# Kernel tuning notes

Measured on AMD Instinct MI355X. Metric: run time of the kernel, lower is better.

## Reference

```python
import jax, jax.numpy as jnp
import numpy as np

DIM = 384
DH = 32
H = DIM // DH          # 12 heads
N_WIN = 3072           # total windows
W_ACT = 1536           # active windows = M
T = 64                 # tokens per window (8x8)
NTOK = W_ACT * T       # 98304 active tokens
N_BLOCK = 9830
MLP = 4 * DIM
EPS = 1e-5


def _layer_norm(h, w, b):
    mu = jnp.mean(h, axis=-1, keepdims=True)
    var = jnp.mean(jnp.square(h - mu), axis=-1, keepdims=True)
    return (h - mu) * jax.lax.rsqrt(var + EPS) * w + b


def setup_inputs() -> dict:
    key = jax.random.key(0)
    ks = jax.random.split(key, 16)
    x = jax.random.normal(ks[0], (N_WIN, T, DIM), jnp.float32)
    # unique active windows, sorted (scatter-restore requires uniqueness)
    index_window = jnp.sort(jax.random.permutation(ks[1], N_WIN)[:W_ACT])
    # full permutation of active tokens into M groups of size S
    index_partition = jax.random.permutation(ks[2], NTOK)
    blocked_index = jax.random.permutation(ks[3], NTOK)[:N_BLOCK]
    s = 0.02
    params = dict(
        ln1_w=jnp.ones((DIM,), jnp.float32), ln1_b=jnp.zeros((DIM,), jnp.float32),
        qkv_w=jax.random.normal(ks[4], (3 * DIM, DIM), jnp.float32) * s,
        qkv_b=jnp.zeros((3 * DIM,), jnp.float32),
        proj_w=jax.random.normal(ks[5], (DIM, DIM), jnp.float32) * s,
        proj_b=jnp.zeros((DIM,), jnp.float32),
        ln2_w=jnp.ones((DIM,), jnp.float32), ln2_b=jnp.zeros((DIM,), jnp.float32),
        fc1_w=jax.random.normal(ks[6], (MLP, DIM), jnp.float32) * s,
        fc1_b=jnp.zeros((MLP,), jnp.float32),
        fc2_w=jax.random.normal(ks[7], (DIM, MLP), jnp.float32) * s,
        fc2_b=jnp.zeros((DIM,), jnp.float32),
    )
    return dict(x=x, index_window=index_window, index_partition=index_partition,
                blocked_index=blocked_index, M=W_ACT, K=jnp.zeros((1,), jnp.int64),
                **params)


def reference(x, index_window, index_partition, blocked_index, M, K,
              ln1_w, ln1_b, qkv_w, qkv_b, proj_w, proj_b,
              ln2_w, ln2_b, fc1_w, fc1_b, fc2_w, fc2_b):
    N, T_, C = x.shape
    scale = DH ** -0.5
    S = index_partition.shape[0] // M

    xn = _layer_norm(x, ln1_w, ln1_b)                      # (N, T, C)
    xw = xn[index_window].reshape(-1, C)                   # (NTOK, C) active tokens
    xp = xw[index_partition].reshape(M, S, C)              # (M, S, C) regrouped
    shortcut = xp

    qkv = (xp @ qkv_w.T + qkv_b).reshape(M, S, H, 3 * DH)  # per-head [q|k|v] chunks
    q, k, v = qkv[..., :DH], qkv[..., DH:2 * DH], qkv[..., 2 * DH:]

    attn = jnp.einsum('mqhd,mkhd->mhqk', q, k) * scale     # (M, H, Sq, Sk)

    # scatter scores into full-size map keyed by KEY token, mask blocked keys, gather back
    amap = jnp.zeros((xw.shape[0], S, H), attn.dtype)      # (NTOK, Sq, H)
    amap = amap.at[index_partition].set(jnp.transpose(attn, (0, 3, 2, 1)).reshape(-1, S, H))
    amap = amap.at[blocked_index].set(-10000.0)
    attn = jnp.transpose(amap[index_partition].reshape(M, S, S, H), (0, 3, 2, 1))
    attn = jax.nn.softmax(attn, axis=-1)

    o = jnp.einsum('mhqk,mkhd->mqhd', attn, v).reshape(M, S, C)
    o = o @ proj_w.T + proj_b

    # sub_layers: [Id, Id(+res), LN, fc1, GELU, fc2(+res)]
    h = shortcut + o
    shortcut = h
    h2 = _layer_norm(h, ln2_w, ln2_b)
    h2 = jax.nn.gelu(h2 @ fc1_w.T + fc1_b, approximate=False)
    h = shortcut + (h2 @ fc2_w.T + fc2_b)

    # scatter-restore: blocked tokens keep their (normed) input values
    XX = xw.at[index_partition].set(h.reshape(-1, C))
    XX = XX.at[blocked_index].set(xw[blocked_index])
    out = xn.at[index_window].set(XX.reshape(M, -1, C))
    return out
```

## Files before the change

### kernel.cpp

```cpp
#include <hip/hip_runtime.h>
#include <hip/hip_bf16.h>

typedef __attribute__((ext_vector_type(8))) short bf16x8;
typedef __attribute__((ext_vector_type(4))) short s16x4;
typedef __attribute__((ext_vector_type(4))) float f32x4;
typedef __attribute__((ext_vector_type(2))) long longx2;
typedef __attribute__((ext_vector_type(16))) unsigned char u8x16;

#define NW_   3072
#define WACT_ 1536
#define NTOK_ 98304
#define NBLK_ 9830
#define DIM_  384
#define QKVD_ 1152
#define MLPD_ 1536

__device__ __forceinline__ float bf2f(short s) {
  union { unsigned u; float f; } c;
  c.u = ((unsigned)(unsigned short)s) << 16;
  return c.f;
}
__device__ __forceinline__ short f2bf(float f) {
  union { float f; unsigned u; } c; c.f = f;
  unsigned lsb = (c.u >> 16) & 1u;
  c.u += 0x7fffu + lsb;
  return (short)(c.u >> 16);
}

__device__ __forceinline__ f32x4 mfma16(bf16x8 a, bf16x8 b, f32x4 c) {
  return __builtin_amdgcn_mfma_f32_16x16x32_bf16(a, b, c, 0, 0, 0);
}
__device__ __forceinline__ f32x4 mfma8(long a, long b, f32x4 c) {
  return __builtin_amdgcn_mfma_f32_16x16x32_fp8_fp8(a, b, c, 0, 0, 0);
}

__device__ __forceinline__ void gload16(const void* g, void* l) {
  __builtin_amdgcn_global_load_lds(
      (const __attribute__((address_space(1))) unsigned*)g,
      (__attribute__((address_space(3))) unsigned*)l, 16, 0, 0);
}

__global__ __launch_bounds__(256) void mapA_k(int* win_rank, unsigned* bitmap) {
  int t = blockIdx.x * 256 + threadIdx.x;
  if (t < NW_) { win_rank[t] = -1; bitmap[t] = 0u; }
}

__global__ __launch_bounds__(256) void mapB_k(const int* __restrict__ iw,
                                              const int* __restrict__ blk,
                                              int* win_rank, unsigned* bitmap) {
  int t = blockIdx.x * 256 + threadIdx.x;
  if (t < WACT_) win_rank[iw[t]] = t;
  if (t < NBLK_) { int j = blk[t]; atomicOr(&bitmap[j >> 5], 1u << (j & 31)); }
}

__global__ __launch_bounds__(256) void mapC_k(const int* __restrict__ ip,
                                              const int* __restrict__ iw,
                                              const unsigned* __restrict__ bitmap,
                                              int* inv_ip, int* rowmap) {
  int i = blockIdx.x * 256 + threadIdx.x;
  if (i < NTOK_) {
    int j = ip[i];
    inv_ip[j] = i;
    int blocked = (bitmap[j >> 5] >> (j & 31)) & 1;
    rowmap[i] = blocked ? -1 : (iw[j >> 6] * 64 + (j & 63));
  }
}

__global__ __launch_bounds__(256) void wconv_k(const float* __restrict__ qkvw,
                                               const float* __restrict__ projw,
                                               const float* __restrict__ fc1w,
                                               short* __restrict__ dst) {
  int i = (blockIdx.x * 256 + threadIdx.x) * 4;
  f32x4 v;
  if (i < 442368) v = *(const f32x4*)&qkvw[i];
  else if (i < 589824) v = *(const f32x4*)&projw[i - 442368];
  else v = *(const f32x4*)&fc1w[i - 589824];
  s16x4 o;
#pragma unroll
  for (int e = 0; e < 4; ++e) o[e] = f2bf(v[e]);
  *(s16x4*)&dst[i] = o;
}

__global__ __launch_bounds__(256) void wconv8_k(const float* __restrict__ fc2w,
                                                unsigned char* __restrict__ dst) {
  int i = (blockIdx.x * 256 + threadIdx.x) * 8;
  f32x4 v0 = *(const f32x4*)&fc2w[i];
  f32x4 v1 = *(const f32x4*)&fc2w[i + 4];
  int w0 = __builtin_amdgcn_cvt_pk_fp8_f32(v0[0], v0[1], 0, false);
  w0 = __builtin_amdgcn_cvt_pk_fp8_f32(v0[2], v0[3], w0, true);
  int w1 = __builtin_amdgcn_cvt_pk_fp8_f32(v1[0], v1[1], 0, false);
  w1 = __builtin_amdgcn_cvt_pk_fp8_f32(v1[2], v1[3], w1, true);
  int kro = i % MLPD_, row = i / MLPD_;
  int g = kro >> 6, l = (kro >> 3) & 7;
  int s = ((l & 3) << 1) | (l >> 2);
  union { int u[2]; long ll; } p; p.u[0] = w0; p.u[1] = w1;
  *(long*)&dst[(size_t)row * MLPD_ + g * 64 + s * 8] = p.ll;
}

__global__ __launch_bounds__(256) void ln1_k(const float* __restrict__ x,
                                             const float* __restrict__ w,
                                             const float* __restrict__ b,
                                             const int* __restrict__ win_rank,
                                             const int* __restrict__ inv_ip,
                                             const unsigned* __restrict__ bitmap,
                                             float* __restrict__ out,
                                             short* __restrict__ xp) {
  const int l = threadIdx.x & 31;
  const int tok = blockIdx.x * 8 + (threadIdx.x >> 5);
  const f32x4* xr = (const f32x4*)(x + (size_t)tok * DIM_);
  f32x4 v[3]; float s = 0.f;
#pragma unroll
  for (int j = 0; j < 3; ++j) {
    v[j] = xr[l + 32 * j];
    s += v[j][0] + v[j][1] + v[j][2] + v[j][3];
  }
#pragma unroll
  for (int m = 1; m <= 16; m <<= 1) s += __shfl_xor(s, m, 64);
  float mu = s * (1.0f / DIM_);
  float q = 0.f;
#pragma unroll
  for (int j = 0; j < 3; ++j)
#pragma unroll
    for (int e = 0; e < 4; ++e) { float d = v[j][e] - mu; q += d * d; }
#pragma unroll
  for (int m = 1; m <= 16; m <<= 1) q += __shfl_xor(q, m, 64);
  float rs = rsqrtf(q * (1.0f / DIM_) + 1e-5f);
  f32x4 y[3];
#pragma unroll
  for (int j = 0; j < 3; ++j) {
    f32x4 wv = *(const f32x4*)&w[4 * l + 128 * j];
    f32x4 bv = *(const f32x4*)&b[4 * l + 128 * j];
#pragma unroll
    for (int e = 0; e < 4; ++e) y[j][e] = (v[j][e] - mu) * rs * wv[e] + bv[e];
  }
  int wdw = tok >> 6, t = tok & 63;
  int rank = win_rank[wdw];
  if (rank < 0) {
    f32x4* po = (f32x4*)(out + (size_t)tok * DIM_);
#pragma unroll
    for (int j = 0; j < 3; ++j) po[l + 32 * j] = y[j];
  } else {
    int jdx = (rank << 6) + t;
    int i = inv_ip[jdx];
#pragma unroll
    for (int j = 0; j < 3; ++j) {
      s16x4 o;
#pragma unroll
      for (int e = 0; e < 4; ++e) o[e] = f2bf(y[j][e]);
      *(s16x4*)&xp[(size_t)i * DIM_ + 4 * l + 128 * j] = o;
    }
    if ((bitmap[jdx >> 5] >> (jdx & 31)) & 1) {
      f32x4* po = (f32x4*)(out + (size_t)tok * DIM_);
#pragma unroll
      for (int j = 0; j < 3; ++j) po[l + 32 * j] = y[j];
    }
  }
}

__global__ __launch_bounds__(256) void ln2_k(const short* __restrict__ h,
                                             const float* __restrict__ w,
                                             const float* __restrict__ b,
                                             short* __restrict__ outln) {
  const int l = threadIdx.x & 31;
  const int tok = blockIdx.x * 8 + (threadIdx.x >> 5);
  const s16x4* xr = (const s16x4*)(h + (size_t)tok * DIM_);
  float v[12]; float s = 0.f;
#pragma unroll
  for (int j = 0; j < 3; ++j) {
    s16x4 rv = xr[l + 32 * j];
#pragma unroll
    for (int e = 0; e < 4; ++e) { v[j * 4 + e] = bf2f(rv[e]); s += v[j * 4 + e]; }
  }
#pragma unroll
  for (int m = 1; m <= 16; m <<= 1) s += __shfl_xor(s, m, 64);
  float mu = s * (1.0f / DIM_);
  float q = 0.f;
#pragma unroll
  for (int e = 0; e < 12; ++e) { float d = v[e] - mu; q += d * d; }
#pragma unroll
  for (int m = 1; m <= 16; m <<= 1) q += __shfl_xor(q, m, 64);
  float rs = rsqrtf(q * (1.0f / DIM_) + 1e-5f);
  s16x4* po = (s16x4*)(outln + (size_t)tok * DIM_);
#pragma unroll
  for (int j = 0; j < 3; ++j) {
    f32x4 wv = *(const f32x4*)&w[4 * l + 128 * j];
    f32x4 bv = *(const f32x4*)&b[4 * l + 128 * j];
    s16x4 o;
#pragma unroll
    for (int e = 0; e < 4; ++e)
      o[e] = f2bf((v[j * 4 + e] - mu) * rs * wv[e] + bv[e]);
    po[l + 32 * j] = o;
  }
}

template <int EPI>
__global__ __launch_bounds__(512) void gemm_k(const short* __restrict__ A,
                                              const short* __restrict__ B,
                                              const float* __restrict__ bias,
                                              int K, int N, int nx,
                                              unsigned char* __restrict__ C8) {
  const int nwg = gridDim.x;
  const int q8 = nwg >> 3;
  const int wg = (blockIdx.x & 7) * q8 + (blockIdx.x >> 3);
  const int ntile = wg % nx, mtile = wg / nx;
  const int tid = threadIdx.x, wid = tid >> 6, lane = tid & 63;
  const int fq = lane >> 4, fr = lane & 15;
  const int wr = wid >> 1, wc = wid & 1;
  __shared__ __align__(16) short lA[256 * 64];
  __shared__ __align__(16) short lB[128 * 64];
  const int row0 = mtile * 256, col0 = ntile * 128;
  float bs[4];
#pragma unroll
  for (int nt = 0; nt < 4; ++nt) bs[nt] = bias[col0 + wc * 64 + nt * 16 + fr];
  f32x4 acc[4][4];
#pragma unroll
  for (int a = 0; a < 4; ++a)
#pragma unroll
    for (int c = 0; c < 4; ++c) acc[a][c] = (f32x4){0.f, 0.f, 0.f, 0.f};
  const int nkt = K >> 6;
  for (int kt = 0; kt < nkt; ++kt) {
    const int k0 = kt << 6;
#pragma unroll
    for (int i = 0; i < 4; ++i) {
      int g = i * 512 + tid;
      int r = g >> 3, c8 = g & 7;
      int s8 = c8 ^ (r & 7);
      gload16(A + (size_t)(row0 + r) * K + k0 + s8 * 8, (char*)lA + (size_t)g * 16);
    }
#pragma unroll
    for (int i = 0; i < 2; ++i) {
      int g = i * 512 + tid;
      int r = g >> 3, c8 = g & 7;
      int s8 = c8 ^ (r & 7);
      gload16(B + (size_t)(col0 + r) * K + k0 + s8 * 8, (char*)lB + (size_t)g * 16);
    }
    __syncthreads();
#pragma unroll
    for (int ks = 0; ks < 2; ++ks) {
      bf16x8 af[4], bfr[4];
#pragma unroll
      for (int mt = 0; mt < 4; ++mt) {
        int r = wr * 64 + mt * 16 + fr;
        af[mt] = *(const bf16x8*)&lA[r * 64 + ((ks * 4 + fq) ^ (r & 7)) * 8];
      }
#pragma unroll
      for (int nt = 0; nt < 4; ++nt) {
        int r = wc * 64 + nt * 16 + fr;
        bfr[nt] = *(const bf16x8*)&lB[r * 64 + ((ks * 4 + fq) ^ (r & 7)) * 8];
      }
#pragma unroll
      for (int mt = 0; mt < 4; ++mt)
#pragma unroll
        for (int nt = 0; nt < 4; ++nt)
          acc[mt][nt] = mfma16(af[mt], bfr[nt], acc[mt][nt]);
    }
    __syncthreads();
  }
#pragma unroll
  for (int mt = 0; mt < 4; ++mt) {
#pragma unroll
    for (int jj = 0; jj < 4; ++jj) {
      int r = row0 + wr * 64 + mt * 16 + fq * 4 + jj;
      if (EPI == 0) {
        float g4[4];
#pragma unroll
        for (int nt = 0; nt < 4; ++nt) g4[nt] = acc[mt][nt][jj] + bs[nt];
        int p01 = __builtin_amdgcn_cvt_pk_fp8_f32(g4[0], g4[1], 0, false);
        int p23 = __builtin_amdgcn_cvt_pk_fp8_f32(g4[2], g4[3], 0, false);
        const size_t rb = (size_t)r * N + col0 + wc * 64 + fr;
        C8[rb]      = (unsigned char)(p01 & 0xff);
        C8[rb + 16] = (unsigned char)((p01 >> 8) & 0xff);
        C8[rb + 32] = (unsigned char)(p23 & 0xff);
        C8[rb + 48] = (unsigned char)((p23 >> 8) & 0xff);
      } else {
        float g4[4];
#pragma unroll
        for (int nt = 0; nt < 4; ++nt) {
          float v = acc[mt][nt][jj] + bs[nt];
          float u = v * (0.79788456f + 0.03567741f * v * v);
          g4[nt] = v * __builtin_amdgcn_rcpf(1.0f + __expf(-2.0f * u));
        }
        int p01 = __builtin_amdgcn_cvt_pk_fp8_f32(g4[0], g4[1], 0, false);
        int p23 = __builtin_amdgcn_cvt_pk_fp8_f32(g4[2], g4[3], 0, false);
        const int C0 = col0 + wc * 64;
        const size_t rb = (size_t)r * MLPD_ + C0 + (fr & 7) + ((fr >> 3) << 4);
        C8[rb]      = (unsigned char)(p01 & 0xff);
        C8[rb + 32] = (unsigned char)((p01 >> 8) & 0xff);
        C8[rb + 8]  = (unsigned char)(p23 & 0xff);
        C8[rb + 40] = (unsigned char)((p23 >> 8) & 0xff);
      }
    }
  }
}

__global__ __launch_bounds__(256) void gemm128_k(const short* __restrict__ A,
                                                 const short* __restrict__ B,
                                                 const float* __restrict__ bias,
                                                 int K, int nx,
                                                 short* __restrict__ Cb,
                                                 const short* __restrict__ add_bf) {
  const int nwg = gridDim.x;
  const int q8 = nwg >> 3;
  const int wg = (blockIdx.x & 7) * q8 + (blockIdx.x >> 3);
  const int ntile = wg % nx, mtile = wg / nx;
  const int tid = threadIdx.x, wid = tid >> 6, lane = tid & 63;
  const int fq = lane >> 4, fr = lane & 15;
  const int wr = wid >> 1, wc = wid & 1;
  __shared__ __align__(16) short lA[128 * 64];
  __shared__ __align__(16) short lB[128 * 64];
  const int row0 = mtile * 128, col0 = ntile * 128;
  float bs[4];
#pragma unroll
  for (int nt = 0; nt < 4; ++nt) bs[nt] = bias[col0 + wc * 64 + nt * 16 + fr];
  f32x4 acc[4][4];
#pragma unroll
  for (int a = 0; a < 4; ++a)
#pragma unroll
    for (int c = 0; c < 4; ++c) acc[a][c] = (f32x4){0.f, 0.f, 0.f, 0.f};
  const int nkt = K >> 6;
  for (int kt = 0; kt < nkt; ++kt) {
    const int k0 = kt << 6;
#pragma unroll
    for (int i = 0; i < 4; ++i) {
      int cb = ((i * 4 + wid) << 6) + lane;
      int r = cb >> 3, c8 = cb & 7;
      int s8 = c8 ^ (r & 7);
      gload16(A + (size_t)(row0 + r) * K + k0 + s8 * 8,
              (char*)lA + (size_t)(i * 4 + wid) * 1024);
      gload16(B + (size_t)(col0 + r) * K + k0 + s8 * 8,
              (char*)lB + (size_t)(i * 4 + wid) * 1024);
    }
    __syncthreads();
#pragma unroll
    for (int ks = 0; ks < 2; ++ks) {
      bf16x8 af[4], bfr[4];
#pragma unroll
      for (int mt = 0; mt < 4; ++mt) {
        int r = wr * 64 + mt * 16 + fr;
        af[mt] = *(const bf16x8*)&lA[r * 64 + ((ks * 4 + fq) ^ (r & 7)) * 8];
      }
#pragma unroll
      for (int nt = 0; nt < 4; ++nt) {
        int r = wc * 64 + nt * 16 + fr;
        bfr[nt] = *(const bf16x8*)&lB[r * 64 + ((ks * 4 + fq) ^ (r & 7)) * 8];
      }
#pragma unroll
      for (int mt = 0; mt < 4; ++mt)
#pragma unroll
        for (int nt = 0; nt < 4; ++nt)
          acc[mt][nt] = mfma16(af[mt], bfr[nt], acc[mt][nt]);
    }
    __syncthreads();
  }
#pragma unroll
  for (int mt = 0; mt < 4; ++mt) {
#pragma unroll
    for (int jj = 0; jj < 4; ++jj) {
      int r = row0 + wr * 64 + mt * 16 + fq * 4 + jj;
#pragma unroll
      for (int nt = 0; nt < 4; ++nt) {
        int gcol = col0 + wc * 64 + nt * 16 + fr;
        float v = acc[mt][nt][jj] + bs[nt] + bf2f(add_bf[(size_t)r * DIM_ + gcol]);
        Cb[(size_t)r * DIM_ + gcol] = f2bf(v);
      }
    }
  }
}

__global__ __launch_bounds__(256) void gemmf8_k(const unsigned char* __restrict__ A8,
                                                const unsigned char* __restrict__ B8,
                                                const float* __restrict__ bias,
                                                int nx,
                                                const short* __restrict__ add_bf,
                                                const int* __restrict__ rowmap,
                                                float* __restrict__ outf) {
  const int K = MLPD_;
  const int nwg = gridDim.x;
  const int q8 = nwg >> 3;
  const int wg = (blockIdx.x & 7) * q8 + (blockIdx.x >> 3);
  const int ntile = wg % nx, mtile = wg / nx;
  const int tid = threadIdx.x, wid = tid >> 6, lane = tid & 63;
  const int fq = lane >> 4, fr = lane & 15;
  const int wr = wid >> 1, wc = wid & 1;
  __shared__ __align__(16) unsigned char lA[128 * 128];
  __shared__ __align__(16) unsigned char lB[128 * 128];
  const int row0 = mtile * 128, col0 = ntile * 128;
  float bs[4];
#pragma unroll
  for (int nt = 0; nt < 4; ++nt) bs[nt] = bias[col0 + wc * 64 + nt * 16 + fr];
  f32x4 acc[4][4];
#pragma unroll
  for (int a = 0; a < 4; ++a)
#pragma unroll
    for (int c = 0; c < 4; ++c) acc[a][c] = (f32x4){0.f, 0.f, 0.f, 0.f};
  const int nkt = K >> 7;
  for (int kt = 0; kt < nkt; ++kt) {
    const int k0 = kt << 7;
#pragma unroll
    for (int i = 0; i < 4; ++i) {
      int g = i * 256 + tid;
      int r = g >> 3, c8 = g & 7;
      int s8 = c8 ^ (r & 7);
      gload16(A8 + (size_t)(row0 + r) * K + k0 + s8 * 16, (char*)lA + (size_t)g * 16);
      gload16(B8 + (size_t)(col0 + r) * K + k0 + s8 * 16, (char*)lB + (size_t)g * 16);
    }
    __syncthreads();
#pragma unroll
    for (int ss = 0; ss < 2; ++ss) {
      longx2 af[4], bfr[4];
      const int pb = ss * 4 + fq;
#pragma unroll
      for (int mt = 0; mt < 4; ++mt) {
        int r = wr * 64 + mt * 16 + fr;
        int d = pb ^ (r & 7);
        af[mt] = *(const longx2*)&lA[r * 128 + d * 16];
      }
#pragma unroll
      for (int nt = 0; nt < 4; ++nt) {
        int r = wc * 64 + nt * 16 + fr;
        int d = pb ^ (r & 7);
        bfr[nt] = *(const longx2*)&lB[r * 128 + d * 16];
      }
#pragma unroll
      for (int mt = 0; mt < 4; ++mt)
#pragma unroll
        for (int nt = 0; nt < 4; ++nt) {
          acc[mt][nt] = mfma8(af[mt][0], bfr[nt][0], acc[mt][nt]);
          acc[mt][nt] = mfma8(af[mt][1], bfr[nt][1], acc[mt][nt]);
        }
    }
    __syncthreads();
  }
#pragma unroll
  for (int mt = 0; mt < 4; ++mt) {
#pragma unroll
    for (int jj = 0; jj < 4; ++jj) {
      int r = row0 + wr * 64 + mt * 16 + fq * 4 + jj;
      int dmap = rowmap[r];
#pragma unroll
      for (int nt = 0; nt < 4; ++nt) {
        int gcol = col0 + wc * 64 + nt * 16 + fr;
        float v = acc[mt][nt][jj] + bs[nt] + bf2f(add_bf[(size_t)r * DIM_ + gcol]);
        if (dmap >= 0) outf[(size_t)dmap * DIM_ + gcol] = v;
      }
    }
  }
}

__global__ __launch_bounds__(256) void attn_k(const unsigned char* __restrict__ qkv8,
                                              const unsigned* __restrict__ bitmap,
                                              const int* __restrict__ ip,
                                              short* __restrict__ o) {
  const int flat = (blockIdx.x & 7) * 576 + (blockIdx.x >> 3);
  const int m = flat / 3;
  const int h = (flat % 3) * 4 + (threadIdx.x >> 6);
  const int wid = threadIdx.x >> 6, lane = threadIdx.x & 63;
  const int fq = lane >> 4, fr = lane & 15;
  __shared__ __align__(16) unsigned char P[4][64 * 72];
  __shared__ __align__(16) unsigned char Vt[4][32 * 72];
  __shared__ unsigned char flags[64];
  if (threadIdx.x < 64) {
    int j = ip[m * 64 + threadIdx.x];
    flags[threadIdx.x] = (unsigned char)((bitmap[j >> 5] >> (j & 31)) & 1);
  }
  __syncthreads();
  const float scale = 0.17677669529663687f;
  int msk[4];
#pragma unroll
  for (int nt = 0; nt < 4; ++nt) msk[nt] = flags[nt * 16 + fr];

  const unsigned char* base = qkv8 + (size_t)m * 64 * QKVD_ + h * 96;
  f32x4 sacc[4][4];
#pragma unroll
  for (int a = 0; a < 4; ++a)
#pragma unroll
    for (int c = 0; c < 4; ++c) sacc[a][c] = (f32x4){0.f, 0.f, 0.f, 0.f};
  long qa[4], kb[4];
#pragma unroll
  for (int mt = 0; mt < 4; ++mt)
    qa[mt] = *(const long*)(base + (size_t)(mt * 16 + fr) * QKVD_ + fq * 8);
#pragma unroll
  for (int nt = 0; nt < 4; ++nt)
    kb[nt] = *(const long*)(base + (size_t)(nt * 16 + fr) * QKVD_ + 32 + fq * 8);
#pragma unroll
  for (int mt = 0; mt < 4; ++mt)
#pragma unroll
    for (int nt = 0; nt < 4; ++nt)
      sacc[mt][nt] = mfma8(qa[mt], kb[nt], sacc[mt][nt]);
#pragma unroll
  for (int c = 0; c < 2; ++c) {
    u8x16 vv = *(const u8x16*)(base + (size_t)lane * QKVD_ + 64 + c * 16);
#pragma unroll
    for (int e = 0; e < 16; ++e) Vt[wid][(c * 16 + e) * 72 + lane] = vv[e];
  }
#pragma unroll
  for (int mt = 0; mt < 4; ++mt)
#pragma unroll
    for (int nt = 0; nt < 4; ++nt) {
      f32x4 sv = sacc[mt][nt];
#pragma unroll
      for (int jj = 0; jj < 4; ++jj)
        sv[jj] = msk[nt] ? -10000.0f : sv[jj] * scale;
      sacc[mt][nt] = sv;
    }
#pragma unroll
  for (int mt = 0; mt < 4; ++mt) {
#pragma unroll
    for (int jj = 0; jj < 4; ++jj) {
      float mx = sacc[mt][0][jj];
#pragma unroll
      for (int nt = 1; nt < 4; ++nt) mx = fmaxf(mx, sacc[mt][nt][jj]);
#pragma unroll
      for (int mm = 1; mm < 16; mm <<= 1) mx = fmaxf(mx, __shfl_xor(mx, mm, 64));
      float sm = 0.f;
      float p[4];
#pragma unroll
      for (int nt = 0; nt < 4; ++nt) {
        p[nt] = __expf(sacc[mt][nt][jj] - mx);
        sm += p[nt];
      }
#pragma unroll
      for (int mm = 1; mm < 16; mm <<= 1) sm += __shfl_xor(sm, mm, 64);
      float inv = 1.0f / sm;
      int rowb = (mt * 16 + fq * 4 + jj) * 72;
      int p01 = __builtin_amdgcn_cvt_pk_fp8_f32(p[0] * inv, p[1] * inv, 0, false);
      int p23 = __builtin_amdgcn_cvt_pk_fp8_f32(p[2] * inv, p[3] * inv, 0, false);
      P[wid][rowb + fr]      = (unsigned char)(p01 & 0xff);
      P[wid][rowb + 16 + fr] = (unsigned char)((p01 >> 8) & 0xff);
      P[wid][rowb + 32 + fr] = (unsigned char)(p23 & 0xff);
      P[wid][rowb + 48 + fr] = (unsigned char)((p23 >> 8) & 0xff);
    }
  }
  f32x4 oacc[4][2];
#pragma unroll
  for (int a = 0; a < 4; ++a)
#pragma unroll
    for (int c = 0; c < 2; ++c) oacc[a][c] = (f32x4){0.f, 0.f, 0.f, 0.f};
#pragma unroll
  for (int ks = 0; ks < 2; ++ks) {
    long pa[4], vb[2];
#pragma unroll
    for (int mt = 0; mt < 4; ++mt)
      pa[mt] = *(const long*)&P[wid][(mt * 16 + fr) * 72 + ks * 32 + fq * 8];
#pragma unroll
    for (int nd = 0; nd < 2; ++nd)
      vb[nd] = *(const long*)&Vt[wid][(nd * 16 + fr) * 72 + ks * 32 + fq * 8];
#pragma unroll
    for (int mt = 0; mt < 4; ++mt)
#pragma unroll
      for (int nd = 0; nd < 2; ++nd)
        oacc[mt][nd] = mfma8(pa[mt], vb[nd], oacc[mt][nd]);
  }
#pragma unroll
  for (int mt = 0; mt < 4; ++mt)
#pragma unroll
    for (int nd = 0; nd < 2; ++nd)
#pragma unroll
      for (int jj = 0; jj < 4; ++jj)
        o[(size_t)(m * 64 + mt * 16 + fq * 4 + jj) * DIM_ + h * 32 + nd * 16 + fr] =
            f2bf(oacc[mt][nd][jj]);
}

extern "C" void kernel_launch(void* const* d_in, const int* in_sizes, int n_in,
                              void* d_out, int out_size, void* d_ws, size_t ws_size,
                              hipStream_t stream) {
  const float* x = (const float*)d_in[0];
  const int* iw = (const int*)d_in[1];
  const int* ip = (const int*)d_in[2];
  const int* blk = (const int*)d_in[3];
  const float* ln1w = (const float*)d_in[6];
  const float* ln1b = (const float*)d_in[7];
  const float* qkvw = (const float*)d_in[8];
  const float* qkvb = (const float*)d_in[9];
  const float* projw = (const float*)d_in[10];
  const float* projb = (const float*)d_in[11];
  const float* ln2w = (const float*)d_in[12];
  const float* ln2b = (const float*)d_in[13];
  const float* fc1w = (const float*)d_in[14];
  const float* fc1b = (const float*)d_in[15];
  const float* fc2w = (const float*)d_in[16];
  const float* fc2b = (const float*)d_in[17];
  float* out = (float*)d_out;

  char* ws = (char*)d_ws;
  short* w_all = (short*)ws;
  short* w_qkv = w_all;
  short* w_proj = w_all + 442368;
  short* w_fc1 = w_all + 589824;
  int* inv_ip = (int*)(ws + 3538944);
  int* rowmap = inv_ip + NTOK_;
  int* win_rank = rowmap + NTOK_;
  unsigned* bitmap = (unsigned*)(win_rank + NW_);
  short* xp = (short*)(ws + 4349952);
  unsigned char* qkv8 = (unsigned char*)(ws + 4349952 + 75497472);
  unsigned char* t8 = qkv8;
  unsigned char* w2f8 = (unsigned char*)(ws + 306339840);
  short* obuf = (short*)(ws + 381837312);
  short* hbuf = (short*)(ws + 457334784);
  short* ln2buf = xp;
  (void)in_sizes; (void)n_in; (void)out_size; (void)ws_size;

  mapA_k<<<12, 256, 0, stream>>>(win_rank, bitmap);
  mapB_k<<<39, 256, 0, stream>>>(iw, blk, win_rank, bitmap);
  mapC_k<<<NTOK_ / 256, 256, 0, stream>>>(ip, iw, bitmap, inv_ip, rowmap);
  wconv_k<<<1152, 256, 0, stream>>>(qkvw, projw, fc1w, w_all);
  wconv8_k<<<288, 256, 0, stream>>>(fc2w, w2f8);
  ln1_k<<<(NW_ * 64) / 8, 256, 0, stream>>>(x, ln1w, ln1b, win_rank, inv_ip, bitmap,
                                            out, xp);
  gemm_k<0><<<384 * 9, 512, 0, stream>>>(xp, w_qkv, qkvb, 384, QKVD_, 9, qkv8);
  attn_k<<<WACT_ * 3, 256, 0, stream>>>(qkv8, bitmap, ip, obuf);
  gemm128_k<<<768 * 3, 256, 0, stream>>>(obuf, w_proj, projb, 384, 3, hbuf, xp);
  ln2_k<<<NTOK_ / 8, 256, 0, stream>>>(hbuf, ln2w, ln2b, ln2buf);
  gemm_k<2><<<384 * 12, 512, 0, stream>>>(ln2buf, w_fc1, fc1b, 384, MLPD_, 12, t8);
  gemmf8_k<<<768 * 3, 256, 0, stream>>>(t8, w2f8, fc2b, 3, hbuf, rowmap, out);
}
```

Baseline: 744.5 us.

## Switch proj and fc1 GEMMs to FP8 with permuted-K activations

Converts the projection and fc1 weights to FP8 with the K-permuted layout, and makes the attention output and LN2 output write FP8 in the same layout. The proj and fc1 GEMMs now use the shared FP8 128x128 GEMM template instead of the bf16 kernels. This halves operand bytes and uses the faster FP8 MFMA path, at the cost of lower precision on two more matmuls. The fc1 tiling changes from 256x128 with 512 threads to 128x128 with 256 threads.

```diff
diff --git a/kernel.cpp b/kernel.cpp
--- a/kernel.cpp
+++ b/kernel.cpp
@@ -38,6 +38,12 @@
   __builtin_amdgcn_global_load_lds(
       (const __attribute__((address_space(1))) unsigned*)g,
       (__attribute__((address_space(3))) unsigned*)l, 16, 0, 0);
+}
+
+__device__ __forceinline__ int kperm(int col) {
+  int l = (col >> 3) & 7;
+  int s = ((l & 3) << 1) | (l >> 2);
+  return (col & ~63) + s * 8 + (col & 7);
 }
 
 __global__ __launch_bounds__(256) void mapA_k(int* win_rank, unsigned* bitmap) {
@@ -67,34 +73,28 @@
 }
 
 __global__ __launch_bounds__(256) void wconv_k(const float* __restrict__ qkvw,
-                                               const float* __restrict__ projw,
-                                               const float* __restrict__ fc1w,
                                                short* __restrict__ dst) {
   int i = (blockIdx.x * 256 + threadIdx.x) * 4;
-  f32x4 v;
-  if (i < 442368) v = *(const f32x4*)&qkvw[i];
-  else if (i < 589824) v = *(const f32x4*)&projw[i - 442368];
-  else v = *(const f32x4*)&fc1w[i - 589824];
+  f32x4 v = *(const f32x4*)&qkvw[i];
   s16x4 o;
 #pragma unroll
   for (int e = 0; e < 4; ++e) o[e] = f2bf(v[e]);
   *(s16x4*)&dst[i] = o;
 }
 
-__global__ __launch_bounds__(256) void wconv8_k(const float* __restrict__ fc2w,
-                                                unsigned char* __restrict__ dst) {
+__global__ __launch_bounds__(256) void wconv8_k(const float* __restrict__ src,
+                                                unsigned char* __restrict__ dst,
+                                                int K) {
   int i = (blockIdx.x * 256 + threadIdx.x) * 8;
-  f32x4 v0 = *(const f32x4*)&fc2w[i];
-  f32x4 v1 = *(const f32x4*)&fc2w[i + 4];
+  f32x4 v0 = *(const f32x4*)&src[i];
+  f32x4 v1 = *(const f32x4*)&src[i + 4];
   int w0 = __builtin_amdgcn_cvt_pk_fp8_f32(v0[0], v0[1], 0, false);
   w0 = __builtin_amdgcn_cvt_pk_fp8_f32(v0[2], v0[3], w0, true);
   int w1 = __builtin_amdgcn_cvt_pk_fp8_f32(v1[0], v1[1], 0, false);
   w1 = __builtin_amdgcn_cvt_pk_fp8_f32(v1[2], v1[3], w1, true);
-  int kro = i % MLPD_, row = i / MLPD_;
-  int g = kro >> 6, l = (kro >> 3) & 7;
-  int s = ((l & 3) << 1) | (l >> 2);
+  int kro = i % K, row = i / K;
   union { int u[2]; long ll; } p; p.u[0] = w0; p.u[1] = w1;
-  *(long*)&dst[(size_t)row * MLPD_ + g * 64 + s * 8] = p.ll;
+  *(long*)&dst[(size_t)row * K + kperm(kro)] = p.ll;
 }
 
 __global__ __launch_bounds__(256) void ln1_k(const float* __restrict__ x,
@@ -160,7 +160,7 @@
 __global__ __launch_bounds__(256) void ln2_k(const short* __restrict__ h,
                                              const float* __restrict__ w,
                                              const float* __restrict__ b,
-                                             short* __restrict__ outln) {
+                                             unsigned char* __restrict__ out8) {
   const int l = threadIdx.x & 31;
   const int tok = blockIdx.x * 8 + (threadIdx.x >> 5);
   const s16x4* xr = (const s16x4*)(h + (size_t)tok * DIM_);
@@ -180,25 +180,26 @@
 #pragma unroll
   for (int m = 1; m <= 16; m <<= 1) q += __shfl_xor(q, m, 64);
   float rs = rsqrtf(q * (1.0f / DIM_) + 1e-5f);
-  s16x4* po = (s16x4*)(outln + (size_t)tok * DIM_);
 #pragma unroll
   for (int j = 0; j < 3; ++j) {
     f32x4 wv = *(const f32x4*)&w[4 * l + 128 * j];
     f32x4 bv = *(const f32x4*)&b[4 * l + 128 * j];
-    s16x4 o;
+    float y[4];
 #pragma unroll
     for (int e = 0; e < 4; ++e)
-      o[e] = f2bf((v[j * 4 + e] - mu) * rs * wv[e] + bv[e]);
-    po[l + 32 * j] = o;
-  }
-}
-
-template <int EPI>
-__global__ __launch_bounds__(512) void gemm_k(const short* __restrict__ A,
-                                              const short* __restrict__ B,
-                                              const float* __restrict__ bias,
-                                              int K, int N, int nx,
-                                              unsigned char* __restrict__ C8) {
+      y[e] = (v[j * 4 + e] - mu) * rs * wv[e] + bv[e];
+    int wrd = __builtin_amdgcn_cvt_pk_fp8_f32(y[0], y[1], 0, false);
+    wrd = __builtin_amdgcn_cvt_pk_fp8_f32(y[2], y[3], wrd, true);
+    int c0 = 4 * l + 128 * j;
+    *(unsigned*)&out8[(size_t)tok * DIM_ + kperm(c0)] = (unsigned)wrd;
+  }
+}
+
+__global__ __launch_bounds__(512) void gemmqkv_k(const short* __restrict__ A,
+                                                 const short* __restrict__ B,
+                                                 const float* __restrict__ bias,
+                                                 unsigned char* __restrict__ C8) {
+  const int K = 384, N = QKVD_, nx = 9;
   const int nwg = gridDim.x;
   const int q8 = nwg >> 3;
   const int wg = (blockIdx.x & 7) * q8 + (blockIdx.x >> 3);
@@ -261,18 +262,101 @@
 #pragma unroll
     for (int jj = 0; jj < 4; ++jj) {
       int r = row0 + wr * 64 + mt * 16 + fq * 4 + jj;
-      if (EPI == 0) {
-        float g4[4];
-#pragma unroll
-        for (int nt = 0; nt < 4; ++nt) g4[nt] = acc[mt][nt][jj] + bs[nt];
-        int p01 = __builtin_amdgcn_cvt_pk_fp8_f32(g4[0], g4[1], 0, false);
-        int p23 = __builtin_amdgcn_cvt_pk_fp8_f32(g4[2], g4[3], 0, false);
-        const size_t rb = (size_t)r * N + col0 + wc * 64 + fr;
-        C8[rb]      = (unsigned char)(p01 & 0xff);
-        C8[rb + 16] = (unsigned char)((p01 >> 8) & 0xff);
-        C8[rb + 32] = (unsigned char)(p23 & 0xff);
-        C8[rb + 48] = (unsigned char)((p23 >> 8) & 0xff);
-      } else {
+      float g4[4];
+#pragma unroll
+      for (int nt = 0; nt < 4; ++nt) g4[nt] = acc[mt][nt][jj] + bs[nt];
+      int p01 = __builtin_amdgcn_cvt_pk_fp8_f32(g4[0], g4[1], 0, false);
+      int p23 = __builtin_amdgcn_cvt_pk_fp8_f32(g4[2], g4[3], 0, false);
+      const size_t rb = (size_t)r * N + col0 + wc * 64 + fr;
+      C8[rb]      = (unsigned char)(p01 & 0xff);
+      C8[rb + 16] = (unsigned char)((p01 >> 8) & 0xff);
+      C8[rb + 32] = (unsigned char)(p23 & 0xff);
+      C8[rb + 48] = (unsigned char)((p23 >> 8) & 0xff);
+    }
+  }
+}
+
+template <int EPI>
+__global__ __launch_bounds__(256) void gemmf8_k(const unsigned char* __restrict__ A8,
+                                                const unsigned char* __restrict__ B8,
+                                                const float* __restrict__ bias,
+                                                int K, int nx,
+                                                short* __restrict__ Cb,
+                                                unsigned char* __restrict__ C8,
+                                                const short* __restrict__ add_bf,
+                                                const int* __restrict__ rowmap,
+                                                float* __restrict__ outf) {
+  const int nwg = gridDim.x;
+  const int q8 = nwg >> 3;
+  const int wg = (blockIdx.x & 7) * q8 + (blockIdx.x >> 3);
+  const int ntile = wg % nx, mtile = wg / nx;
+  const int tid = threadIdx.x, wid = tid >> 6, lane = tid & 63;
+  const int fq = lane >> 4, fr = lane & 15;
+  const int wr = wid >> 1, wc = wid & 1;
+  __shared__ __align__(16) unsigned char lA[128 * 128];
+  __shared__ __align__(16) unsigned char lB[128 * 128];
+  const int row0 = mtile * 128, col0 = ntile * 128;
+  float bs[4];
+#pragma unroll
+  for (int nt = 0; nt < 4; ++nt) bs[nt] = bias[col0 + wc * 64 + nt * 16 + fr];
+  f32x4 acc[4][4];
+#pragma unroll
+  for (int a = 0; a < 4; ++a)
+#pragma unroll
+    for (int c = 0; c < 4; ++c) acc[a][c] = (f32x4){0.f, 0.f, 0.f, 0.f};
+  const int nkt = K >> 7;
+  for (int kt = 0; kt < nkt; ++kt) {
+    const int k0 = kt << 7;
+#pragma unroll
+    for (int i = 0; i < 4; ++i) {
+      int g = i * 256 + tid;
+      int r = g >> 3, c8 = g & 7;
+      int s8 = c8 ^ (r & 7);
+      gload16(A8 + (size_t)(row0 + r) * K + k0 + s8 * 16, (char*)lA + (size_t)g * 16);
+      gload16(B8 + (size_t)(col0 + r) * K + k0 + s8 * 16, (char*)lB + (size_t)g * 16);
+    }
+    __syncthreads();
+#pragma unroll
+    for (int ss = 0; ss < 2; ++ss) {
+      longx2 af[4], bfr[4];
+      const int pb = ss * 4 + fq;
+#pragma unroll
+      for (int mt = 0; mt < 4; ++mt) {
+        int r = wr * 64 + mt * 16 + fr;
+        int d = pb ^ (r & 7);
+        af[mt] = *(const longx2*)&lA[r * 128 + d * 16];
+      }
+#pragma unroll
+      for (int nt = 0; nt < 4; ++nt) {
+        int r = wc * 64 + nt * 16 + fr;
+        int d = pb ^ (r & 7);
+        bfr[nt] = *(const longx2*)&lB[r * 128 + d * 16];
+      }
+#pragma unroll
+      for (int mt = 0; mt < 4; ++mt)
+#pragma unroll
+        for (int nt = 0; nt < 4; ++nt) {
+          acc[mt][nt] = mfma8(af[mt][0], bfr[nt][0], acc[mt][nt]);
+          acc[mt][nt] = mfma8(af[mt][1], bfr[nt][1], acc[mt][nt]);
+        }
+    }
+    __syncthreads();
+  }
+#pragma unroll
+  for (int mt = 0; mt < 4; ++mt) {
+#pragma unroll
+    for (int jj = 0; jj < 4; ++jj) {
+      int r = row0 + wr * 64 + mt * 16 + fq * 4 + jj;
+      int dmap = 0;
+      if (EPI == 3) dmap = rowmap[r];
+      if (EPI == 1) {
+#pragma unroll
+        for (int nt = 0; nt < 4; ++nt) {
+          int gcol = col0 + wc * 64 + nt * 16 + fr;
+          float v = acc[mt][nt][jj] + bs[nt] + bf2f(add_bf[(size_t)r * DIM_ + gcol]);
+          Cb[(size_t)r * DIM_ + gcol] = f2bf(v);
+        }
+      } else if (EPI == 2) {
         float g4[4];
 #pragma unroll
         for (int nt = 0; nt < 4; ++nt) {
@@ -288,160 +372,13 @@
         C8[rb + 32] = (unsigned char)((p01 >> 8) & 0xff);
         C8[rb + 8]  = (unsigned char)(p23 & 0xff);
         C8[rb + 40] = (unsigned char)((p23 >> 8) & 0xff);
-      }
-    }
-  }
-}
-
-__global__ __launch_bounds__(256) void gemm128_k(const short* __restrict__ A,
-                                                 const short* __restrict__ B,
-                                                 const float* __restrict__ bias,
-                                                 int K, int nx,
-                                                 short* __restrict__ Cb,
-                                                 const short* __restrict__ add_bf) {
-  const int nwg = gridDim.x;
-  const int q8 = nwg >> 3;
-  const int wg = (blockIdx.x & 7) * q8 + (blockIdx.x >> 3);
-  const int ntile = wg % nx, mtile = wg / nx;
-  const int tid = threadIdx.x, wid = tid >> 6, lane = tid & 63;
-  const int fq = lane >> 4, fr = lane & 15;
-  const int wr = wid >> 1, wc = wid & 1;
-  __shared__ __align__(16) short lA[128 * 64];
-  __shared__ __align__(16) short lB[128 * 64];
-  const int row0 = mtile * 128, col0 = ntile * 128;
-  float bs[4];
-#pragma unroll
-  for (int nt = 0; nt < 4; ++nt) bs[nt] = bias[col0 + wc * 64 + nt * 16 + fr];
-  f32x4 acc[4][4];
-#pragma unroll
-  for (int a = 0; a < 4; ++a)
-#pragma unroll
-    for (int c = 0; c < 4; ++c) acc[a][c] = (f32x4){0.f, 0.f, 0.f, 0.f};
-  const int nkt = K >> 6;
-  for (int kt = 0; kt < nkt; ++kt) {
-    const int k0 = kt << 6;
-#pragma unroll
-    for (int i = 0; i < 4; ++i) {
-      int cb = ((i * 4 + wid) << 6) + lane;
-      int r = cb >> 3, c8 = cb & 7;
-      int s8 = c8 ^ (r & 7);
-      gload16(A + (size_t)(row0 + r) * K + k0 + s8 * 8,
-              (char*)lA + (size_t)(i * 4 + wid) * 1024);
-      gload16(B + (size_t)(col0 + r) * K + k0 + s8 * 8,
-              (char*)lB + (size_t)(i * 4 + wid) * 1024);
-    }
-    __syncthreads();
-#pragma unroll
-    for (int ks = 0; ks < 2; ++ks) {
-      bf16x8 af[4], bfr[4];
-#pragma unroll
-      for (int mt = 0; mt < 4; ++mt) {
-        int r = wr * 64 + mt * 16 + fr;
-        af[mt] = *(const bf16x8*)&lA[r * 64 + ((ks * 4 + fq) ^ (r & 7)) * 8];
-      }
-#pragma unroll
-      for (int nt = 0; nt < 4; ++nt) {
-        int r = wc * 64 + nt * 16 + fr;
-        bfr[nt] = *(const bf16x8*)&lB[r * 64 + ((ks * 4 + fq) ^ (r & 7)) * 8];
-      }
-#pragma unroll
-      for (int mt = 0; mt < 4; ++mt)
-#pragma unroll
-        for (int nt = 0; nt < 4; ++nt)
-          acc[mt][nt] = mfma16(af[mt], bfr[nt], acc[mt][nt]);
-    }
-    __syncthreads();
-  }
-#pragma unroll
-  for (int mt = 0; mt < 4; ++mt) {
-#pragma unroll
-    for (int jj = 0; jj < 4; ++jj) {
-      int r = row0 + wr * 64 + mt * 16 + fq * 4 + jj;
-#pragma unroll
-      for (int nt = 0; nt < 4; ++nt) {
-        int gcol = col0 + wc * 64 + nt * 16 + fr;
-        float v = acc[mt][nt][jj] + bs[nt] + bf2f(add_bf[(size_t)r * DIM_ + gcol]);
-        Cb[(size_t)r * DIM_ + gcol] = f2bf(v);
-      }
-    }
-  }
-}
-
-__global__ __launch_bounds__(256) void gemmf8_k(const unsigned char* __restrict__ A8,
-                                                const unsigned char* __restrict__ B8,
-                                                const float* __restrict__ bias,
-                                                int nx,
-                                                const short* __restrict__ add_bf,
-                                                const int* __restrict__ rowmap,
-                                                float* __restrict__ outf) {
-  const int K = MLPD_;
-  const int nwg = gridDim.x;
-  const int q8 = nwg >> 3;
-  const int wg = (blockIdx.x & 7) * q8 + (blockIdx.x >> 3);
-  const int ntile = wg % nx, mtile = wg / nx;
-  const int tid = threadIdx.x, wid = tid >> 6, lane = tid & 63;
-  const int fq = lane >> 4, fr = lane & 15;
-  const int wr = wid >> 1, wc = wid & 1;
-  __shared__ __align__(16) unsigned char lA[128 * 128];
-  __shared__ __align__(16) unsigned char lB[128 * 128];
-  const int row0 = mtile * 128, col0 = ntile * 128;
-  float bs[4];
-#pragma unroll
-  for (int nt = 0; nt < 4; ++nt) bs[nt] = bias[col0 + wc * 64 + nt * 16 + fr];
-  f32x4 acc[4][4];
-#pragma unroll
-  for (int a = 0; a < 4; ++a)
-#pragma unroll
-    for (int c = 0; c < 4; ++c) acc[a][c] = (f32x4){0.f, 0.f, 0.f, 0.f};
-  const int nkt = K >> 7;
-  for (int kt = 0; kt < nkt; ++kt) {
-    const int k0 = kt << 7;
-#pragma unroll
-    for (int i = 0; i < 4; ++i) {
-      int g = i * 256 + tid;
-      int r = g >> 3, c8 = g & 7;
-      int s8 = c8 ^ (r & 7);
-      gload16(A8 + (size_t)(row0 + r) * K + k0 + s8 * 16, (char*)lA + (size_t)g * 16);
-      gload16(B8 + (size_t)(col0 + r) * K + k0 + s8 * 16, (char*)lB + (size_t)g * 16);
-    }
-    __syncthreads();
-#pragma unroll
-    for (int ss = 0; ss < 2; ++ss) {
-      longx2 af[4], bfr[4];
-      const int pb = ss * 4 + fq;
-#pragma unroll
-      for (int mt = 0; mt < 4; ++mt) {
-        int r = wr * 64 + mt * 16 + fr;
-        int d = pb ^ (r & 7);
-        af[mt] = *(const longx2*)&lA[r * 128 + d * 16];
-      }
-#pragma unroll
-      for (int nt = 0; nt < 4; ++nt) {
-        int r = wc * 64 + nt * 16 + fr;
-        int d = pb ^ (r & 7);
-        bfr[nt] = *(const longx2*)&lB[r * 128 + d * 16];
-      }
-#pragma unroll
-      for (int mt = 0; mt < 4; ++mt)
+      } else {
 #pragma unroll
         for (int nt = 0; nt < 4; ++nt) {
-          acc[mt][nt] = mfma8(af[mt][0], bfr[nt][0], acc[mt][nt]);
-          acc[mt][nt] = mfma8(af[mt][1], bfr[nt][1], acc[mt][nt]);
+          int gcol = col0 + wc * 64 + nt * 16 + fr;
+          float v = acc[mt][nt][jj] + bs[nt] + bf2f(add_bf[(size_t)r * DIM_ + gcol]);
+          if (dmap >= 0) outf[(size_t)dmap * DIM_ + gcol] = v;
         }
-    }
-    __syncthreads();
-  }
-#pragma unroll
-  for (int mt = 0; mt < 4; ++mt) {
-#pragma unroll
-    for (int jj = 0; jj < 4; ++jj) {
-      int r = row0 + wr * 64 + mt * 16 + fq * 4 + jj;
-      int dmap = rowmap[r];
-#pragma unroll
-      for (int nt = 0; nt < 4; ++nt) {
-        int gcol = col0 + wc * 64 + nt * 16 + fr;
-        float v = acc[mt][nt][jj] + bs[nt] + bf2f(add_bf[(size_t)r * DIM_ + gcol]);
-        if (dmap >= 0) outf[(size_t)dmap * DIM_ + gcol] = v;
       }
     }
   }
@@ -450,7 +387,7 @@
 __global__ __launch_bounds__(256) void attn_k(const unsigned char* __restrict__ qkv8,
                                               const unsigned* __restrict__ bitmap,
                                               const int* __restrict__ ip,
-                                              short* __restrict__ o) {
+                                              unsigned char* __restrict__ o8) {
   const int flat = (blockIdx.x & 7) * 576 + (blockIdx.x >> 3);
   const int m = flat / 3;
   const int h = (flat % 3) * 4 + (threadIdx.x >> 6);
@@ -551,14 +488,18 @@
       for (int nd = 0; nd < 2; ++nd)
         oacc[mt][nd] = mfma8(pa[mt], vb[nd], oacc[mt][nd]);
   }
+  const int pos0 = kperm(h * 32 + fr);
+  const int pos1 = kperm(h * 32 + 16 + fr);
 #pragma unroll
   for (int mt = 0; mt < 4; ++mt)
 #pragma unroll
-    for (int nd = 0; nd < 2; ++nd)
-#pragma unroll
-      for (int jj = 0; jj < 4; ++jj)
-        o[(size_t)(m * 64 + mt * 16 + fq * 4 + jj) * DIM_ + h * 32 + nd * 16 + fr] =
-            f2bf(oacc[mt][nd][jj]);
+    for (int jj = 0; jj < 4; ++jj) {
+      int p01 = __builtin_amdgcn_cvt_pk_fp8_f32(oacc[mt][0][jj], oacc[mt][1][jj],
+                                                0, false);
+      size_t rb = (size_t)(m * 64 + mt * 16 + fq * 4 + jj) * DIM_;
+      o8[rb + pos0] = (unsigned char)(p01 & 0xff);
+      o8[rb + pos1] = (unsigned char)((p01 >> 8) & 0xff);
+    }
 }
 
 extern "C" void kernel_launch(void* const* d_in, const int* in_sizes, int n_in,
@@ -583,34 +524,38 @@
   float* out = (float*)d_out;
 
   char* ws = (char*)d_ws;
-  short* w_all = (short*)ws;
-  short* w_qkv = w_all;
-  short* w_proj = w_all + 442368;
-  short* w_fc1 = w_all + 589824;
-  int* inv_ip = (int*)(ws + 3538944);
+  short* w_qkv = (short*)ws;
+  unsigned char* projw8 = (unsigned char*)(ws + 884736);
+  unsigned char* fc1w8 = (unsigned char*)(ws + 1032192);
+  unsigned char* fc2w8 = (unsigned char*)(ws + 1622016);
+  int* inv_ip = (int*)(ws + 2211840);
   int* rowmap = inv_ip + NTOK_;
   int* win_rank = rowmap + NTOK_;
   unsigned* bitmap = (unsigned*)(win_rank + NW_);
   short* xp = (short*)(ws + 4349952);
-  unsigned char* qkv8 = (unsigned char*)(ws + 4349952 + 75497472);
+  unsigned char* qkv8 = (unsigned char*)(ws + 79847424);
   unsigned char* t8 = qkv8;
-  unsigned char* w2f8 = (unsigned char*)(ws + 306339840);
-  short* obuf = (short*)(ws + 381837312);
+  unsigned char* obuf8 = (unsigned char*)(ws + 306339840);
+  unsigned char* ln2buf8 = (unsigned char*)(ws + 344088576);
   short* hbuf = (short*)(ws + 457334784);
-  short* ln2buf = xp;
   (void)in_sizes; (void)n_in; (void)out_size; (void)ws_size;
 
   mapA_k<<<12, 256, 0, stream>>>(win_rank, bitmap);
   mapB_k<<<39, 256, 0, stream>>>(iw, blk, win_rank, bitmap);
   mapC_k<<<NTOK_ / 256, 256, 0, stream>>>(ip, iw, bitmap, inv_ip, rowmap);
-  wconv_k<<<1152, 256, 0, stream>>>(qkvw, projw, fc1w, w_all);
-  wconv8_k<<<288, 256, 0, stream>>>(fc2w, w2f8);
+  wconv_k<<<432, 256, 0, stream>>>(qkvw, w_qkv);
+  wconv8_k<<<72, 256, 0, stream>>>(projw, projw8, 384);
+  wconv8_k<<<288, 256, 0, stream>>>(fc1w, fc1w8, 384);
+  wconv8_k<<<288, 256, 0, stream>>>(fc2w, fc2w8, MLPD_);
   ln1_k<<<(NW_ * 64) / 8, 256, 0, stream>>>(x, ln1w, ln1b, win_rank, inv_ip, bitmap,
                                             out, xp);
-  gemm_k<0><<<384 * 9, 512, 0, stream>>>(xp, w_qkv, qkvb, 384, QKVD_, 9, qkv8);
-  attn_k<<<WACT_ * 3, 256, 0, stream>>>(qkv8, bitmap, ip, obuf);
-  gemm128_k<<<768 * 3, 256, 0, stream>>>(obuf, w_proj, projb, 384, 3, hbuf, xp);
-  ln2_k<<<NTOK_ / 8, 256, 0, stream>>>(hbuf, ln2w, ln2b, ln2buf);
-  gemm_k<2><<<384 * 12, 512, 0, stream>>>(ln2buf, w_fc1, fc1b, 384, MLPD_, 12, t8);
-  gemmf8_k<<<768 * 3, 256, 0, stream>>>(t8, w2f8, fc2b, 3, hbuf, rowmap, out);
-}
+  gemmqkv_k<<<384 * 9, 512, 0, stream>>>(xp, w_qkv, qkvb, qkv8);
+  attn_k<<<WACT_ * 3, 256, 0, stream>>>(qkv8, bitmap, ip, obuf8);
+  gemmf8_k<1><<<768 * 3, 256, 0, stream>>>(obuf8, projw8, projb, 384, 3, hbuf,
+                                           nullptr, xp, nullptr, nullptr);
+  ln2_k<<<NTOK_ / 8, 256, 0, stream>>>(hbuf, ln2w, ln2b, ln2buf8);
+  gemmf8_k<2><<<768 * 12, 256, 0, stream>>>(ln2buf8, fc1w8, fc1b, 384, 12, nullptr,
+                                            t8, nullptr, nullptr, nullptr);
+  gemmf8_k<3><<<768 * 3, 256, 0, stream>>>(t8, fc2w8, fc2b, MLPD_, 3, nullptr,
+                                           nullptr, hbuf, rowmap, out);
+}
```

After: 704.0 us. 1.06x faster.
